# Kernel optimization log

Hardware: AMD Instinct MI355X
Metric: run time of the kernel (lower is better)

The kernel has to match this reference:

```python
import jax, jax.numpy as jnp
import numpy as np

EPS = 1e-7  # Keras K.epsilon()
ATT_DIM = 50

def setup_inputs() -> dict:
    key = jax.random.key(0)
    k1, k2, k3, k4 = jax.random.split(key, 4)
    B, T, D = 64, 4096, 256
    x = jax.random.normal(k1, (B, T, D), dtype=jnp.float32)
    # RandomNormal init (stddev default 0.05 in keras RandomNormal)
    W = 0.05 * jax.random.normal(k2, (D, ATT_DIM), dtype=jnp.float32)
    b = 0.05 * jax.random.normal(k3, (ATT_DIM,), dtype=jnp.float32)
    u = 0.05 * jax.random.normal(k4, (ATT_DIM, 1), dtype=jnp.float32)
    return {"x": x, "W": W, "b": b, "u": u}

def reference(x, W, b, u):
    # uit: [B, T, A]
    uit = jnp.tanh(jnp.einsum('btd,da->bta', x, W) + b)
    # ait: [B, T]  (no max-subtraction, faithful to K.exp then normalize)
    ait = jnp.exp(jnp.einsum('bta,a->bt', uit, u[:, 0]))
    ait = ait / (jnp.sum(ait, axis=1, keepdims=True) + EPS)
    # weighted sum pooling over seq axis -> [B, D]
    return jnp.einsum('btd,bt->bd', x, ait)
```

## Files before the change

kernel.cpp:

```cpp
#include <hip/hip_runtime.h>
#include <stdint.h>

#define B_    64
#define T_    4096
#define D_    256
#define A_    50
#define APAD  64
#define TB    256
#define ST    32
#define WT_STRIDE 264
#define XS_STRIDE 264
#define EPS_  1e-7f

#define OFF_NUM 0
#define OFF_DEN 16384
#define OFF_B   16448
#define OFF_U   16512
#define OFF_WT  16576

typedef __attribute__((ext_vector_type(8))) short short8;
typedef __attribute__((ext_vector_type(4))) float floatx4;

__device__ __forceinline__ unsigned short f32_to_bf16(float f) {
    union { float f; uint32_t u; } v; v.f = f;
    uint32_t u = v.u;
    uint32_t r = u + 0x7FFFu + ((u >> 16) & 1u);
    return (unsigned short)(r >> 16);
}

__device__ __forceinline__ float fast_tanh(float x) {
    float e2 = __expf(2.0f * x);
    return (e2 - 1.0f) * __builtin_amdgcn_rcpf(e2 + 1.0f);
}

__global__ void att_prologue(const float* __restrict__ W,
                             const float* __restrict__ bias,
                             const float* __restrict__ u,
                             float* __restrict__ ws) {
    int idx = blockIdx.x * blockDim.x + threadIdx.x;
    int stride = gridDim.x * blockDim.x;
    for (int i = idx; i < OFF_DEN + B_; i += stride) ws[i] = 0.0f;
    for (int i = idx; i < APAD; i += stride) {
        ws[OFF_B + i] = (i < A_) ? bias[i] : 0.0f;
        ws[OFF_U + i] = (i < A_) ? u[i]    : 0.0f;
    }
    unsigned short* wt = (unsigned short*)(ws + OFF_WT);
    for (int i = idx; i < APAD * D_; i += stride) {
        int a = i >> 8;
        int k = i & 255;
        float val = (a < A_) ? W[k * A_ + a] : 0.0f;
        wt[a * WT_STRIDE + k] = f32_to_bf16(val);
    }
}

__global__ __launch_bounds__(256) void att_main(const float* __restrict__ x,
                                                float* __restrict__ ws) {
    __shared__ unsigned short lds_wt[APAD * WT_STRIDE];
    __shared__ unsigned short lds_x[ST * XS_STRIDE];
    __shared__ float part[ST][2];
    __shared__ float e_lds[ST];

    const int tid  = threadIdx.x;
    const int wave = tid >> 6;
    const int lane = tid & 63;
    const int bb   = blockIdx.y;
    const int tblk = blockIdx.x;

    const float* xblk = x + ((size_t)bb * T_ + (size_t)tblk * TB) * D_;

    float4 r[8];
    {
        const float4* xg = (const float4*)xblk;
        #pragma unroll
        for (int i = 0; i < 8; ++i) r[i] = xg[tid + (i << 8)];
    }

    {
        const uint4* g = (const uint4*)(ws + OFF_WT);
        uint4* l = (uint4*)lds_wt;
        for (int i = tid; i < (APAD * WT_STRIDE * 2) / 16; i += 256) l[i] = g[i];
    }

    const int mt  = wave & 1;
    const int nt0 = (wave >> 1) * 2, nt1 = nt0 + 1;
    const int c0  = nt0 * 16 + (lane & 15);
    const int c1  = nt1 * 16 + (lane & 15);
    const float b0 = ws[OFF_B + c0], b1 = ws[OFF_B + c1];
    const float u0 = ws[OFF_U + c0], u1 = ws[OFF_U + c1];

    float num_acc = 0.0f;
    float den_acc = 0.0f;

    const int arow_off = (mt * 16 + (lane & 15)) * XS_STRIDE;
    const int koff     = (lane >> 4) * 8;
    const int brow0    = (nt0 * 16 + (lane & 15)) * WT_STRIDE;
    const int brow1    = (nt1 * 16 + (lane & 15)) * WT_STRIDE;

    for (int st = 0; st < TB / ST; ++st) {
        __syncthreads();

        #pragma unroll
        for (int i = 0; i < 8; ++i) {
            int f = tid + (i << 8);
            int row = f >> 6;
            int col4 = f & 63;
            uint32_t p0 = ((uint32_t)f32_to_bf16(r[i].y) << 16) | f32_to_bf16(r[i].x);
            uint32_t p1 = ((uint32_t)f32_to_bf16(r[i].w) << 16) | f32_to_bf16(r[i].z);
            uint32_t* dst = (uint32_t*)&lds_x[row * XS_STRIDE + col4 * 4];
            dst[0] = p0; dst[1] = p1;
        }
        __syncthreads();

        if (st < TB / ST - 1) {
            const float4* xn = (const float4*)(xblk + (st + 1) * ST * D_);
            #pragma unroll
            for (int i = 0; i < 8; ++i) r[i] = xn[tid + (i << 8)];
        }

        floatx4 acc0 = {0.f, 0.f, 0.f, 0.f};
        floatx4 acc1 = {0.f, 0.f, 0.f, 0.f};
        #pragma unroll
        for (int ks = 0; ks < 8; ++ks) {
            short8 a  = *(const short8*)&lds_x[arow_off + ks * 32 + koff];
            short8 w0 = *(const short8*)&lds_wt[brow0 + ks * 32 + koff];
            short8 w1 = *(const short8*)&lds_wt[brow1 + ks * 32 + koff];
            acc0 = __builtin_amdgcn_mfma_f32_16x16x32_bf16(a, w0, acc0, 0, 0, 0);
            acc1 = __builtin_amdgcn_mfma_f32_16x16x32_bf16(a, w1, acc1, 0, 0, 0);
        }

        float lp[4];
        #pragma unroll
        for (int rr = 0; rr < 4; ++rr) {
            float v0 = fast_tanh(acc0[rr] + b0) * u0;
            float v1 = fast_tanh(acc1[rr] + b1) * u1;
            float v = v0 + v1;
            v += __shfl_xor(v, 1);
            v += __shfl_xor(v, 2);
            v += __shfl_xor(v, 4);
            v += __shfl_xor(v, 8);
            lp[rr] = v;
        }
        if ((lane & 15) == 0) {
            int rg = lane >> 4;
            #pragma unroll
            for (int rr = 0; rr < 4; ++rr)
                part[mt * 16 + rg * 4 + rr][wave >> 1] = lp[rr];
        }
        __syncthreads();

        if (tid < ST) {
            float ev = __expf(part[tid][0] + part[tid][1]);
            e_lds[tid] = ev;
            den_acc += ev;
        }
        __syncthreads();

        #pragma unroll
        for (int t = 0; t < ST; ++t) {
            float xv = __uint_as_float((uint32_t)lds_x[t * XS_STRIDE + tid] << 16);
            num_acc = fmaf(xv, e_lds[t], num_acc);
        }
    }

    atomicAdd(&ws[OFF_NUM + bb * D_ + tid], num_acc);
    if (wave == 0) {
        float v = den_acc;
        v += __shfl_xor(v, 32);
        v += __shfl_xor(v, 16);
        v += __shfl_xor(v, 8);
        v += __shfl_xor(v, 4);
        v += __shfl_xor(v, 2);
        v += __shfl_xor(v, 1);
        if (lane == 0) atomicAdd(&ws[OFF_DEN + bb], v);
    }
}

__global__ void att_epilogue(const float* __restrict__ ws, float* __restrict__ out) {
    int bb = blockIdx.x;
    int d  = threadIdx.x;
    out[bb * D_ + d] = ws[OFF_NUM + bb * D_ + d] / (ws[OFF_DEN + bb] + EPS_);
}

extern "C" void kernel_launch(void* const* d_in, const int* in_sizes, int n_in,
                              void* d_out, int out_size, void* d_ws, size_t ws_size,
                              hipStream_t stream) {
    const float* x = (const float*)d_in[0];
    const float* W = (const float*)d_in[1];
    const float* b = (const float*)d_in[2];
    const float* u = (const float*)d_in[3];
    float* ws  = (float*)d_ws;
    float* out = (float*)d_out;

    att_prologue<<<64, 256, 0, stream>>>(W, b, u, ws);
    att_main<<<dim3(T_ / TB, B_), 256, 0, stream>>>(x, ws);
    att_epilogue<<<B_, 256, 0, stream>>>(ws, out);
}
```

Before: 369.8 us.

## Keep W tile in registers per wave and drop LDS W staging

Each wave now owns one 16-column slice of the attention dimension and holds its bf16 W fragments in registers for the whole kernel, instead of copying the full padded W into LDS and re-reading it every sub-tile. The wave split changes from (M-tile, N-pair) to per-N-tile with both M-tiles, so the partial-score buffer grows to four columns. The x staging writes are widened to 16-byte LDS stores, and launch bounds request 4 blocks per CU. This removes about 33KB of LDS per block and the per-step W LDS reads, raising occupancy, at the cost of extra VGPRs for the W fragments and more shuffle work per wave.

```diff
diff --git a/kernel.cpp b/kernel.cpp
--- a/kernel.cpp
+++ b/kernel.cpp
@@ -53,11 +53,10 @@
     }
 }
 
-__global__ __launch_bounds__(256) void att_main(const float* __restrict__ x,
-                                                float* __restrict__ ws) {
-    __shared__ unsigned short lds_wt[APAD * WT_STRIDE];
+__global__ __launch_bounds__(256, 4) void att_main(const float* __restrict__ x,
+                                                   float* __restrict__ ws) {
     __shared__ unsigned short lds_x[ST * XS_STRIDE];
-    __shared__ float part[ST][2];
+    __shared__ float part[ST][4];
     __shared__ float e_lds[ST];
 
     const int tid  = threadIdx.x;
@@ -72,84 +71,90 @@
     {
         const float4* xg = (const float4*)xblk;
         #pragma unroll
-        for (int i = 0; i < 8; ++i) r[i] = xg[tid + (i << 8)];
-    }
-
+        for (int i = 0; i < 4; ++i) {
+            r[2 * i]     = xg[2 * tid + 512 * i];
+            r[2 * i + 1] = xg[2 * tid + 512 * i + 1];
+        }
+    }
+
+    short8 bw[8];
     {
-        const uint4* g = (const uint4*)(ws + OFF_WT);
-        uint4* l = (uint4*)lds_wt;
-        for (int i = tid; i < (APAD * WT_STRIDE * 2) / 16; i += 256) l[i] = g[i];
-    }
-
-    const int mt  = wave & 1;
-    const int nt0 = (wave >> 1) * 2, nt1 = nt0 + 1;
-    const int c0  = nt0 * 16 + (lane & 15);
-    const int c1  = nt1 * 16 + (lane & 15);
-    const float b0 = ws[OFF_B + c0], b1 = ws[OFF_B + c1];
-    const float u0 = ws[OFF_U + c0], u1 = ws[OFF_U + c1];
+        const unsigned short* wt = (const unsigned short*)(ws + OFF_WT);
+        const unsigned short* wrow = wt + (wave * 16 + (lane & 15)) * WT_STRIDE
+                                        + ((lane >> 4) * 8);
+        #pragma unroll
+        for (int ks = 0; ks < 8; ++ks)
+            bw[ks] = *(const short8*)(wrow + ks * 32);
+    }
+
+    const int c = wave * 16 + (lane & 15);
+    const float b_c = ws[OFF_B + c];
+    const float u_c = ws[OFF_U + c];
 
     float num_acc = 0.0f;
     float den_acc = 0.0f;
 
-    const int arow_off = (mt * 16 + (lane & 15)) * XS_STRIDE;
-    const int koff     = (lane >> 4) * 8;
-    const int brow0    = (nt0 * 16 + (lane & 15)) * WT_STRIDE;
-    const int brow1    = (nt1 * 16 + (lane & 15)) * WT_STRIDE;
+    const int arow0 = (lane & 15) * XS_STRIDE;
+    const int arow1 = (16 + (lane & 15)) * XS_STRIDE;
+    const int koff  = (lane >> 4) * 8;
+    const int wrow_lds = (tid >> 5) * XS_STRIDE + (tid & 31) * 8;
 
     for (int st = 0; st < TB / ST; ++st) {
         __syncthreads();
 
         #pragma unroll
-        for (int i = 0; i < 8; ++i) {
-            int f = tid + (i << 8);
-            int row = f >> 6;
-            int col4 = f & 63;
-            uint32_t p0 = ((uint32_t)f32_to_bf16(r[i].y) << 16) | f32_to_bf16(r[i].x);
-            uint32_t p1 = ((uint32_t)f32_to_bf16(r[i].w) << 16) | f32_to_bf16(r[i].z);
-            uint32_t* dst = (uint32_t*)&lds_x[row * XS_STRIDE + col4 * 4];
-            dst[0] = p0; dst[1] = p1;
+        for (int i = 0; i < 4; ++i) {
+            uint4 p;
+            p.x = ((uint32_t)f32_to_bf16(r[2*i].y)   << 16) | f32_to_bf16(r[2*i].x);
+            p.y = ((uint32_t)f32_to_bf16(r[2*i].w)   << 16) | f32_to_bf16(r[2*i].z);
+            p.z = ((uint32_t)f32_to_bf16(r[2*i+1].y) << 16) | f32_to_bf16(r[2*i+1].x);
+            p.w = ((uint32_t)f32_to_bf16(r[2*i+1].w) << 16) | f32_to_bf16(r[2*i+1].z);
+            *(uint4*)&lds_x[wrow_lds + i * 8 * XS_STRIDE] = p;
         }
         __syncthreads();
 
         if (st < TB / ST - 1) {
             const float4* xn = (const float4*)(xblk + (st + 1) * ST * D_);
             #pragma unroll
-            for (int i = 0; i < 8; ++i) r[i] = xn[tid + (i << 8)];
+            for (int i = 0; i < 4; ++i) {
+                r[2 * i]     = xn[2 * tid + 512 * i];
+                r[2 * i + 1] = xn[2 * tid + 512 * i + 1];
+            }
         }
 
         floatx4 acc0 = {0.f, 0.f, 0.f, 0.f};
         floatx4 acc1 = {0.f, 0.f, 0.f, 0.f};
         #pragma unroll
         for (int ks = 0; ks < 8; ++ks) {
-            short8 a  = *(const short8*)&lds_x[arow_off + ks * 32 + koff];
-            short8 w0 = *(const short8*)&lds_wt[brow0 + ks * 32 + koff];
-            short8 w1 = *(const short8*)&lds_wt[brow1 + ks * 32 + koff];
-            acc0 = __builtin_amdgcn_mfma_f32_16x16x32_bf16(a, w0, acc0, 0, 0, 0);
-            acc1 = __builtin_amdgcn_mfma_f32_16x16x32_bf16(a, w1, acc1, 0, 0, 0);
-        }
-
-        float lp[4];
+            short8 a0 = *(const short8*)&lds_x[arow0 + ks * 32 + koff];
+            short8 a1 = *(const short8*)&lds_x[arow1 + ks * 32 + koff];
+            acc0 = __builtin_amdgcn_mfma_f32_16x16x32_bf16(a0, bw[ks], acc0, 0, 0, 0);
+            acc1 = __builtin_amdgcn_mfma_f32_16x16x32_bf16(a1, bw[ks], acc1, 0, 0, 0);
+        }
+
+        float lp0[4], lp1[4];
         #pragma unroll
         for (int rr = 0; rr < 4; ++rr) {
-            float v0 = fast_tanh(acc0[rr] + b0) * u0;
-            float v1 = fast_tanh(acc1[rr] + b1) * u1;
-            float v = v0 + v1;
-            v += __shfl_xor(v, 1);
-            v += __shfl_xor(v, 2);
-            v += __shfl_xor(v, 4);
-            v += __shfl_xor(v, 8);
-            lp[rr] = v;
+            float v0 = fast_tanh(acc0[rr] + b_c) * u_c;
+            float v1 = fast_tanh(acc1[rr] + b_c) * u_c;
+            v0 += __shfl_xor(v0, 1); v1 += __shfl_xor(v1, 1);
+            v0 += __shfl_xor(v0, 2); v1 += __shfl_xor(v1, 2);
+            v0 += __shfl_xor(v0, 4); v1 += __shfl_xor(v1, 4);
+            v0 += __shfl_xor(v0, 8); v1 += __shfl_xor(v1, 8);
+            lp0[rr] = v0; lp1[rr] = v1;
         }
         if ((lane & 15) == 0) {
             int rg = lane >> 4;
             #pragma unroll
-            for (int rr = 0; rr < 4; ++rr)
-                part[mt * 16 + rg * 4 + rr][wave >> 1] = lp[rr];
+            for (int rr = 0; rr < 4; ++rr) {
+                part[rg * 4 + rr][wave]      = lp0[rr];
+                part[16 + rg * 4 + rr][wave] = lp1[rr];
+            }
         }
         __syncthreads();
 
         if (tid < ST) {
-            float ev = __expf(part[tid][0] + part[tid][1]);
+            float ev = __expf(part[tid][0] + part[tid][1] + part[tid][2] + part[tid][3]);
             e_lds[tid] = ev;
             den_acc += ev;
         }
```

Result: no change. 366.7 us (-0.8%).
